# Kernel optimization log

Measured on AMD Instinct MI355X. Metric: run time of the kernel, lower is better.

Reference implementation:

```python
import jax, jax.numpy as jnp
import numpy as np

N = 100000
E = 1600000
D = 64
EPS = 1e-5


def setup_inputs() -> dict:
    key = jax.random.key(0)
    ks = jax.random.split(key, 16)
    x = jax.random.normal(ks[0], (N, D), dtype=jnp.float32)
    edge_index = jax.random.randint(ks[1], (2, E), 0, N, dtype=jnp.int64)
    s = 1.0 / np.sqrt(D)
    params = {
        'W1': jax.random.uniform(ks[2], (D, D), jnp.float32, -s, s),
        'b1': jnp.zeros((D,), jnp.float32),
        'g1': jnp.ones((D,), jnp.float32),
        'be1': jnp.zeros((D,), jnp.float32),
        'W2': jax.random.uniform(ks[3], (D, D), jnp.float32, -s, s),
        'b2': jnp.zeros((D,), jnp.float32),
        'g2': jnp.ones((D,), jnp.float32),
        'be2': jnp.zeros((D,), jnp.float32),
        'W3': jax.random.uniform(ks[4], (D, D), jnp.float32, -s, s),
        'b3': jnp.zeros((D,), jnp.float32),
    }
    return {'x': x, 'edge_index': edge_index, **params}


def _gcn_norm(edge_index):
    # add self-loops, symmetric normalization (PyG GCNConv default)
    loop = jnp.arange(N, dtype=edge_index.dtype)
    src = jnp.concatenate([edge_index[0], loop])  # [E+N]
    dst = jnp.concatenate([edge_index[1], loop])
    deg = jax.ops.segment_sum(jnp.ones_like(src, dtype=jnp.float32), dst, num_segments=N)
    dinv = jnp.where(deg > 0, jax.lax.rsqrt(deg), 0.0)
    norm = dinv[src] * dinv[dst]  # [E+N]
    return src, dst, norm


def _gcn_conv(x, src, dst, norm, W, b):
    h = x @ W                        # [N, D] transform first (PyG order)
    msg = h[src] * norm[:, None]     # gather + scale  [E+N, D]
    out = jax.ops.segment_sum(msg, dst, num_segments=N)  # scatter-add
    return out + b


def _bn(x, g, b):
    # BatchNorm1d over nodes, batch statistics (training-mode math)
    m = jnp.mean(x, axis=0)
    v = jnp.var(x, axis=0)
    return g * (x - m) * jax.lax.rsqrt(v + EPS) + b


def reference(x, edge_index, W1, b1, g1, be1, W2, b2, g2, be2, W3, b3):
    src, dst, norm = _gcn_norm(edge_index)
    h = _gcn_conv(x, src, dst, norm, W1, b1)
    h = jax.nn.relu(_bn(h, g1, be1))
    h = _gcn_conv(h, src, dst, norm, W2, b2)
    h = jax.nn.relu(_bn(h, g2, be2))
    h = _gcn_conv(h, src, dst, norm, W3, b3)
    return h
```

## Files before the change

kernel.cpp:

```cpp
#include <hip/hip_runtime.h>
#include <hip/hip_bf16.h>


#define FD 64
#define EPSF 1e-5f

#define NBUCK 256
#define BSHIFT 9
#define BWID 512
#define SLOTS 28
#define P1_EDGES 4096

typedef __attribute__((ext_vector_type(8))) short bf16x8;
typedef __attribute__((ext_vector_type(4))) float f32x4;

__device__ __forceinline__ float bf2f(ushort u) {
  return __uint_as_float((unsigned)u << 16);
}
__device__ __forceinline__ ushort f2bf_bits(float f) {
  __hip_bfloat16 h = __float2bfloat16(f);
  return *(ushort*)&h;
}

__global__ void detect64_kernel(const int* __restrict__ ei, int* __restrict__ flag) {
  int lane = threadIdx.x;
  int v = ei[2 * lane + 1];
  unsigned long long nz = __ballot(v != 0);
  if (lane == 0) *flag = (nz == 0ull) ? 1 : 0;
}

__global__ __launch_bounds__(256) void hist_kernel(const int* __restrict__ ei, int E,
                                                   const int* __restrict__ flag,
                                                   int* __restrict__ bhist) {
  __shared__ int h[NBUCK];
  const int tid = threadIdx.x;
  h[tid] = 0;
  __syncthreads();
  const int is64 = *flag;
  const int base = blockIdx.x * P1_EDGES;
#pragma unroll 1
  for (int k = 0; k < P1_EDGES / 256; ++k) {
    int e = base + k * 256 + tid;
    if (e < E) {
      int d = is64 ? ei[2 * (E + e)] : ei[E + e];
      atomicAdd(&h[d >> BSHIFT], 1);
    }
  }
  __syncthreads();
  if (h[tid]) atomicAdd(&bhist[tid], h[tid]);
}

__global__ __launch_bounds__(256) void bscan_kernel(const int* __restrict__ bhist,
                                                    int* __restrict__ bbase,
                                                    int* __restrict__ bcur) {
  __shared__ int lds[NBUCK];
  int t = threadIdx.x;
  int v = bhist[t];
  lds[t] = v;
  __syncthreads();
  for (int off = 1; off < NBUCK; off <<= 1) {
    int tv = (t >= off) ? lds[t - off] : 0;
    __syncthreads();
    lds[t] += tv;
    __syncthreads();
  }
  int ex = lds[t] - v;
  bbase[t] = ex;
  bcur[t] = ex;
}

__global__ __launch_bounds__(256) void fill1_kernel(const int* __restrict__ ei, int E,
                                                    const int* __restrict__ flag,
                                                    int* __restrict__ bcur,
                                                    int2* __restrict__ stage) {
  __shared__ int2 sbuf[NBUCK][SLOTS];
  __shared__ int scnt[NBUCK];
  __shared__ int sbase[NBUCK];
  const int tid = threadIdx.x;
  scnt[tid] = 0;
  __syncthreads();
  const int is64 = *flag;
  const int base = blockIdx.x * P1_EDGES;
#pragma unroll 1
  for (int k = 0; k < P1_EDGES / 256; ++k) {
    int e = base + k * 256 + tid;
    if (e < E) {
      int s = is64 ? ei[2 * e] : ei[e];
      int d = is64 ? ei[2 * (E + e)] : ei[E + e];
      int b = d >> BSHIFT;
      int pos = atomicAdd(&scnt[b], 1);
      if (pos < SLOTS) {
        sbuf[b][pos] = make_int2(s, d);
      } else {
        stage[atomicAdd(&bcur[b], 1)] = make_int2(s, d);
      }
    }
  }
  __syncthreads();
  {
    int c = scnt[tid];
    if (c > SLOTS) c = SLOTS;
    scnt[tid] = c;
    sbase[tid] = c ? atomicAdd(&bcur[tid], c) : 0;
  }
  __syncthreads();
  for (int idx = tid; idx < NBUCK * SLOTS; idx += 256) {
    int b = idx / SLOTS, sl = idx - b * SLOTS;
    if (sl < scnt[b]) stage[sbase[b] + sl] = sbuf[b][sl];
  }
}

__global__ __launch_bounds__(256) void degcount_kernel(const int2* __restrict__ stage,
                                                       const int* __restrict__ bbase,
                                                       const int* __restrict__ bcur,
                                                       int* __restrict__ deg,
                                                       float* __restrict__ dinv, int N) {
  __shared__ int h[BWID];
  const int b = blockIdx.x;
  const int tid = threadIdx.x;
  for (int i = tid; i < BWID; i += 256) h[i] = 0;
  __syncthreads();
  const int lo = bbase[b], hi = bcur[b];
  for (int i = lo + tid; i < hi; i += 256)
    atomicAdd(&h[stage[i].y - (b << BSHIFT)], 1);
  __syncthreads();
  const int n0 = b << BSHIFT;
  for (int i = tid; i < BWID; i += 256) {
    int node = n0 + i;
    if (node < N) {
      int d = h[i];
      deg[node] = d;
      dinv[node] = rsqrtf((float)(d + 1));
    }
  }
}

__global__ __launch_bounds__(1024) void scan1_kernel(const int* __restrict__ deg,
                                                     int* __restrict__ rowptr,
                                                     int* __restrict__ partial, int N) {
  __shared__ int lds[1024];
  int i = blockIdx.x * 1024 + threadIdx.x;
  int v = (i < N) ? deg[i] : 0;
  lds[threadIdx.x] = v;
  __syncthreads();
  for (int off = 1; off < 1024; off <<= 1) {
    int t = (threadIdx.x >= (unsigned)off) ? lds[threadIdx.x - off] : 0;
    __syncthreads();
    lds[threadIdx.x] += t;
    __syncthreads();
  }
  if (i < N) rowptr[i + 1] = lds[threadIdx.x];
  if (threadIdx.x == 1023) partial[blockIdx.x] = lds[1023];
}

__global__ __launch_bounds__(128) void scan2_kernel(int* __restrict__ partial, int B) {
  __shared__ int lds[128];
  int t = threadIdx.x;
  int v = (t < B) ? partial[t] : 0;
  lds[t] = v;
  __syncthreads();
  for (int off = 1; off < 128; off <<= 1) {
    int tv = (t >= off) ? lds[t - off] : 0;
    __syncthreads();
    lds[t] += tv;
    __syncthreads();
  }
  if (t < B) partial[t] = lds[t] - v;
}

__global__ __launch_bounds__(1024) void scan3_kernel(const int* __restrict__ deg,
                                                     int* __restrict__ rowptr,
                                                     const int* __restrict__ partial,
                                                     int* __restrict__ cursor, int N) {
  int i = blockIdx.x * 1024 + threadIdx.x;
  if (i < N) {
    int r = rowptr[i + 1] + partial[blockIdx.x];
    rowptr[i + 1] = r;
    cursor[i] = r - deg[i];
    if (i == 0) rowptr[0] = 0;
  }
}

__global__ __launch_bounds__(256) void fill2_kernel(const int2* __restrict__ stage,
                                                    const int* __restrict__ bbase,
                                                    const int* __restrict__ bcur,
                                                    int* __restrict__ cursor,
                                                    const float* __restrict__ dinv,
                                                    int2* __restrict__ colw) {
  const int b = blockIdx.x >> 1;
  const int half = blockIdx.x & 1;
  const int lo = bbase[b];
  const int hi = bcur[b];
  for (int i = lo + half * 256 + threadIdx.x; i < hi; i += 512) {
    int2 sd = stage[i];
    int slot = atomicAdd(&cursor[sd.y], 1);
    colw[slot] = make_int2(sd.x, __float_as_int(dinv[sd.x] * dinv[sd.y]));
  }
}

__global__ __launch_bounds__(256) void deg_atomic_kernel(const int* __restrict__ ei, int E,
                                                         const int* __restrict__ flag,
                                                         int* __restrict__ deg) {
  int e = blockIdx.x * 256 + threadIdx.x;
  if (e >= E) return;
  const int is64 = *flag;
  int d = is64 ? ei[2 * (E + e)] : ei[E + e];
  atomicAdd(&deg[d], 1);
}
__global__ __launch_bounds__(256) void dinv_kernel(const int* __restrict__ deg,
                                                   float* __restrict__ dinv, int N) {
  int i = blockIdx.x * 256 + threadIdx.x;
  if (i < N) dinv[i] = rsqrtf((float)(deg[i] + 1));
}
__global__ __launch_bounds__(256) void fill_direct_kernel(const int* __restrict__ ei, int E,
                                                          const int* __restrict__ flag,
                                                          const float* __restrict__ dinv,
                                                          int* __restrict__ cursor,
                                                          int2* __restrict__ colw) {
  int e = blockIdx.x * 256 + threadIdx.x;
  if (e >= E) return;
  const int is64 = *flag;
  int s = is64 ? ei[2 * e] : ei[e];
  int d = is64 ? ei[2 * (E + e)] : ei[E + e];
  int slot = atomicAdd(&cursor[d], 1);
  colw[slot] = make_int2(s, __float_as_int(dinv[s] * dinv[d]));
}

__global__ __launch_bounds__(256) void cast_kernel(const float* __restrict__ in,
                                                   ushort* __restrict__ out, int total) {
  int i = (blockIdx.x * 256 + threadIdx.x) * 4;
  if (i >= total) return;
  float4 v = *(const float4*)(in + i);
  ushort4 o;
  o.x = f2bf_bits(v.x);
  o.y = f2bf_bits(v.y);
  o.z = f2bf_bits(v.z);
  o.w = f2bf_bits(v.w);
  *(ushort4*)(out + i) = o;
}

template <bool BN>
__global__ __launch_bounds__(256) void agg_kernel(const ushort* __restrict__ H,
                                                  const int* __restrict__ rowptr,
                                                  const int2* __restrict__ colw,
                                                  const float* __restrict__ dinv,
                                                  const float* __restrict__ stats,
                                                  const float* __restrict__ g,
                                                  const float* __restrict__ be,
                                                  ushort* __restrict__ out, int N) {
  const int lane = threadIdx.x & 63;
  const int wid = threadIdx.x >> 6;
  const int dst = blockIdx.x * 4 + wid;
  if (dst >= N) return;

  float a = 1.f, c = 0.f;
  if (BN) {
    float invN = 1.0f / (float)N;
    float m = stats[lane] * invN;
    float v = stats[64 + lane] * invN - m * m;
    float r = rsqrtf(v + EPSF);
    a = g[lane] * r;
    c = be[lane] - m * a;
  }

  const float di = dinv[dst];
  float hd = bf2f(H[(size_t)dst * FD + lane]);
  if (BN) hd = fmaxf(fmaf(a, hd, c), 0.f);
  const float self = di * di * hd;

  float acc[8] = {0.f, 0.f, 0.f, 0.f, 0.f, 0.f, 0.f, 0.f};

  const int e0 = __builtin_amdgcn_readfirstlane(rowptr[dst]);
  const int e1 = __builtin_amdgcn_readfirstlane(rowptr[dst + 1]);
  for (int e = e0; e < e1; e += 8) {
#pragma unroll
    for (int u = 0; u < 8; ++u) {
      int ee = e + u;
      int idx = (ee < e1) ? ee : (e1 - 1);
      int2 cw = colw[idx];
      float w = (ee < e1) ? __int_as_float(cw.y) : 0.f;
      float h = bf2f(H[(size_t)cw.x * FD + lane]);
      if (BN) h = fmaxf(fmaf(a, h, c), 0.f);
      acc[u] = fmaf(w, h, acc[u]);
    }
  }
  float s = ((acc[0] + acc[1]) + (acc[2] + acc[3])) +
            ((acc[4] + acc[5]) + (acc[6] + acc[7])) + self;
  out[(size_t)dst * FD + lane] = f2bf_bits(s);
}

template <bool BF16OUT>
__global__ __launch_bounds__(256) void gemm_mfma_kernel(const ushort* __restrict__ A,
                                                        const float* __restrict__ W,
                                                        const float* __restrict__ bias,
                                                        ushort* __restrict__ outb,
                                                        float* __restrict__ outf,
                                                        float* __restrict__ stats, int N) {
  const int lane = threadIdx.x & 63;
  const int wid = threadIdx.x >> 6;
  const int lo = lane & 15;
  const int hi = lane >> 4;

  __shared__ float sred[128];
  if (BF16OUT) {
    if (threadIdx.x < 128) sred[threadIdx.x] = 0.f;
    __syncthreads();
  }

  bf16x8 bfrag[2][4];
#pragma unroll
  for (int kk = 0; kk < 2; ++kk)
#pragma unroll
    for (int nt = 0; nt < 4; ++nt)
#pragma unroll
      for (int j = 0; j < 8; ++j) {
        int k = kk * 32 + hi * 8 + j;
        bfrag[kk][nt][j] = (short)f2bf_bits(W[k * FD + nt * 16 + lo]);
      }

  float bl[4];
#pragma unroll
  for (int nt = 0; nt < 4; ++nt) bl[nt] = bias[nt * 16 + lo];

  float s1[4] = {0.f, 0.f, 0.f, 0.f};
  float s2[4] = {0.f, 0.f, 0.f, 0.f};

  const int TILES = (N + 15) / 16;
  const int stride = gridDim.x * 4;
  for (int tile = blockIdx.x * 4 + wid; tile < TILES; tile += stride) {
    const int row0 = tile * 16;
    const int ar = min(row0 + lo, N - 1);
    const ushort* ap = A + (size_t)ar * FD + hi * 8;
    bf16x8 a0 = *(const bf16x8*)ap;
    bf16x8 a1 = *(const bf16x8*)(ap + 32);

    f32x4 acc[4] = {{0.f, 0.f, 0.f, 0.f},
                    {0.f, 0.f, 0.f, 0.f},
                    {0.f, 0.f, 0.f, 0.f},
                    {0.f, 0.f, 0.f, 0.f}};
#pragma unroll
    for (int nt = 0; nt < 4; ++nt) {
      acc[nt] = __builtin_amdgcn_mfma_f32_16x16x32_bf16(a0, bfrag[0][nt], acc[nt], 0, 0, 0);
      acc[nt] = __builtin_amdgcn_mfma_f32_16x16x32_bf16(a1, bfrag[1][nt], acc[nt], 0, 0, 0);
    }

#pragma unroll
    for (int nt = 0; nt < 4; ++nt) {
#pragma unroll
      for (int r = 0; r < 4; ++r) {
        int row = row0 + hi * 4 + r;
        if (row < N) {
          float o = acc[nt][r] + bl[nt];
          if (BF16OUT) {
            outb[(size_t)row * FD + nt * 16 + lo] = f2bf_bits(o);
            s1[nt] += o;
            s2[nt] += o * o;
          } else {
            outf[(size_t)row * FD + nt * 16 + lo] = o;
          }
        }
      }
    }
  }

  if (BF16OUT) {
#pragma unroll
    for (int nt = 0; nt < 4; ++nt) {
      atomicAdd(&sred[nt * 16 + lo], s1[nt]);
      atomicAdd(&sred[64 + nt * 16 + lo], s2[nt]);
    }
    __syncthreads();
    if (threadIdx.x < 128) atomicAdd(&stats[threadIdx.x], sred[threadIdx.x]);
  }
}

extern "C" void kernel_launch(void* const* d_in, const int* in_sizes, int n_in,
                              void* d_out, int out_size, void* d_ws, size_t ws_size,
                              hipStream_t stream) {
  const float* x = (const float*)d_in[0];
  const int* ei = (const int*)d_in[1];
  const float* W1 = (const float*)d_in[2];
  const float* b1 = (const float*)d_in[3];
  const float* g1 = (const float*)d_in[4];
  const float* be1 = (const float*)d_in[5];
  const float* W2 = (const float*)d_in[6];
  const float* b2 = (const float*)d_in[7];
  const float* g2 = (const float*)d_in[8];
  const float* be2 = (const float*)d_in[9];
  const float* W3 = (const float*)d_in[10];
  const float* b3 = (const float*)d_in[11];

  const int N = in_sizes[0] / FD;
  const int E = in_sizes[1] / 2;
  const int nB = (N + BWID - 1) >> BSHIFT;

  char* p = (char*)d_ws;
  auto alloc = [&](size_t bytes) {
    char* r = p;
    p += (bytes + 255) & ~(size_t)255;
    return r;
  };
  int* flag = (int*)alloc(4);
  float* stats1 = (float*)alloc(128 * 4);
  float* stats2 = (float*)alloc(128 * 4);
  int* partial = (int*)alloc(128 * 4);
  int* bhist = (int*)alloc(NBUCK * 4);
  int* bbase = (int*)alloc(NBUCK * 4);
  int* bcur = (int*)alloc(NBUCK * 4);
  int* deg = (int*)alloc((size_t)N * 4);
  float* dinv = (float*)alloc((size_t)N * 4);
  int* rowptr = (int*)alloc((size_t)(N + 1) * 4);
  int* cursor = (int*)alloc((size_t)N * 4);
  int2* colw = (int2*)alloc((size_t)E * 8);
  ushort* T0 = (ushort*)alloc((size_t)N * FD * 2);
  ushort* T1 = (ushort*)alloc((size_t)N * FD * 2);
  size_t base_need = (size_t)(p - (char*)d_ws);
  int2* stage = (int2*)alloc((size_t)E * 8);
  size_t full_need = (size_t)(p - (char*)d_ws);
  const bool two_phase =
      ((ws_size == 0) || (ws_size >= full_need)) && (N <= NBUCK * BWID);
  (void)base_need;

  hipMemsetAsync(stats1, 0, 128 * 4, stream);
  hipMemsetAsync(stats2, 0, 128 * 4, stream);

  const int NB = (N + 1023) / 1024;
  const int EB = (E + P1_EDGES - 1) / P1_EDGES;

  detect64_kernel<<<1, 64, 0, stream>>>(ei, flag);

  if (two_phase) {
    hipMemsetAsync(bhist, 0, NBUCK * 4, stream);
    hist_kernel<<<EB, 256, 0, stream>>>(ei, E, flag, bhist);
    bscan_kernel<<<1, NBUCK, 0, stream>>>(bhist, bbase, bcur);
    fill1_kernel<<<EB, 256, 0, stream>>>(ei, E, flag, bcur, stage);
    degcount_kernel<<<nB, 256, 0, stream>>>(stage, bbase, bcur, deg, dinv, N);
    scan1_kernel<<<NB, 1024, 0, stream>>>(deg, rowptr, partial, N);
    scan2_kernel<<<1, 128, 0, stream>>>(partial, NB);
    scan3_kernel<<<NB, 1024, 0, stream>>>(deg, rowptr, partial, cursor, N);
    fill2_kernel<<<2 * nB, 256, 0, stream>>>(stage, bbase, bcur, cursor, dinv, colw);
  } else {
    hipMemsetAsync(deg, 0, (size_t)N * 4, stream);
    deg_atomic_kernel<<<(E + 255) / 256, 256, 0, stream>>>(ei, E, flag, deg);
    dinv_kernel<<<(N + 255) / 256, 256, 0, stream>>>(deg, dinv, N);
    scan1_kernel<<<NB, 1024, 0, stream>>>(deg, rowptr, partial, N);
    scan2_kernel<<<1, 128, 0, stream>>>(partial, NB);
    scan3_kernel<<<NB, 1024, 0, stream>>>(deg, rowptr, partial, cursor, N);
    fill_direct_kernel<<<(E + 255) / 256, 256, 0, stream>>>(ei, E, flag, dinv, cursor,
                                                            colw);
  }

  const int aggGrid = (N + 3) / 4;
  const int castGrid = (N * FD / 4 + 255) / 256;
  const int TILES = (N + 15) / 16;
  const int gemmGrid = (TILES + 15) / 16;

  cast_kernel<<<castGrid, 256, 0, stream>>>(x, T0, N * FD);
  agg_kernel<false><<<aggGrid, 256, 0, stream>>>(T0, rowptr, colw, dinv, nullptr, nullptr,
                                                 nullptr, T1, N);
  gemm_mfma_kernel<true><<<gemmGrid, 256, 0, stream>>>(T1, W1, b1, T0, nullptr, stats1, N);

  agg_kernel<true><<<aggGrid, 256, 0, stream>>>(T0, rowptr, colw, dinv, stats1, g1, be1,
                                                T1, N);
  gemm_mfma_kernel<true><<<gemmGrid, 256, 0, stream>>>(T1, W2, b2, T0, nullptr, stats2, N);

  agg_kernel<true><<<aggGrid, 256, 0, stream>>>(T0, rowptr, colw, dinv, stats2, g2, be2,
                                                T1, N);
  gemm_mfma_kernel<false><<<gemmGrid, 256, 0, stream>>>(T1, W3, b3, nullptr,
                                                        (float*)d_out, nullptr, N);
}
```

Baseline: 351.4 us.

## Aggregate four nodes per wavefront with 16 lanes each; fold memsets into init kernel

The aggregation kernel now gives each 16-lane group one destination node, with each lane loading 4 bf16 features (8 bytes) per neighbour instead of 2 bytes per lane for a whole wavefront per node. The goal is wider per-lane gathers, fewer waves, and per-group loop bounds under an __any loop. Because the four nodes in a wave have different degrees, groups that finish early sit idle until the longest row is done. The separate memsets and the detect kernel are also merged into one init kernel to cut launch overhead.

```diff
diff --git a/kernel.cpp b/kernel.cpp
--- a/kernel.cpp
+++ b/kernel.cpp
@@ -22,11 +22,22 @@
   return *(ushort*)&h;
 }
 
-__global__ void detect64_kernel(const int* __restrict__ ei, int* __restrict__ flag) {
-  int lane = threadIdx.x;
-  int v = ei[2 * lane + 1];
-  unsigned long long nz = __ballot(v != 0);
-  if (lane == 0) *flag = (nz == 0ull) ? 1 : 0;
+__global__ __launch_bounds__(256) void init_kernel(const int* __restrict__ ei,
+                                                   int* __restrict__ flag,
+                                                   int* __restrict__ bhist,
+                                                   float* __restrict__ stats1,
+                                                   float* __restrict__ stats2) {
+  int t = threadIdx.x;
+  bhist[t] = 0;
+  if (t < 128) {
+    stats1[t] = 0.f;
+    stats2[t] = 0.f;
+  }
+  if (t < 64) {
+    int v = ei[2 * t + 1];
+    unsigned long long nz = __ballot(v != 0);
+    if (t == 0) *flag = (nz == 0ull) ? 1 : 0;
+  }
 }
 
 __global__ __launch_bounds__(256) void hist_kernel(const int* __restrict__ ei, int E,
@@ -250,43 +261,89 @@
                                                   ushort* __restrict__ out, int N) {
   const int lane = threadIdx.x & 63;
   const int wid = threadIdx.x >> 6;
-  const int dst = blockIdx.x * 4 + wid;
-  if (dst >= N) return;
-
-  float a = 1.f, c = 0.f;
+  const int grp = lane >> 4;
+  const int fl = lane & 15;
+  const int dst = (blockIdx.x * 4 + wid) * 4 + grp;
+  const bool live = dst < N;
+  const int dc = live ? dst : N - 1;
+
+  float a[4], cc[4];
   if (BN) {
-    float invN = 1.0f / (float)N;
-    float m = stats[lane] * invN;
-    float v = stats[64 + lane] * invN - m * m;
-    float r = rsqrtf(v + EPSF);
-    a = g[lane] * r;
-    c = be[lane] - m * a;
-  }
-
-  const float di = dinv[dst];
-  float hd = bf2f(H[(size_t)dst * FD + lane]);
-  if (BN) hd = fmaxf(fmaf(a, hd, c), 0.f);
-  const float self = di * di * hd;
-
-  float acc[8] = {0.f, 0.f, 0.f, 0.f, 0.f, 0.f, 0.f, 0.f};
-
-  const int e0 = __builtin_amdgcn_readfirstlane(rowptr[dst]);
-  const int e1 = __builtin_amdgcn_readfirstlane(rowptr[dst + 1]);
-  for (int e = e0; e < e1; e += 8) {
-#pragma unroll
-    for (int u = 0; u < 8; ++u) {
-      int ee = e + u;
-      int idx = (ee < e1) ? ee : (e1 - 1);
-      int2 cw = colw[idx];
-      float w = (ee < e1) ? __int_as_float(cw.y) : 0.f;
-      float h = bf2f(H[(size_t)cw.x * FD + lane]);
-      if (BN) h = fmaxf(fmaf(a, h, c), 0.f);
-      acc[u] = fmaf(w, h, acc[u]);
-    }
-  }
-  float s = ((acc[0] + acc[1]) + (acc[2] + acc[3])) +
-            ((acc[4] + acc[5]) + (acc[6] + acc[7])) + self;
-  out[(size_t)dst * FD + lane] = f2bf_bits(s);
+    const float invN = 1.0f / (float)N;
+#pragma unroll
+    for (int j = 0; j < 4; ++j) {
+      int f = fl * 4 + j;
+      float m = stats[f] * invN;
+      float v = stats[64 + f] * invN - m * m;
+      float r = rsqrtf(v + EPSF);
+      a[j] = g[f] * r;
+      cc[j] = be[f] - m * a[j];
+    }
+  }
+
+  const int e0 = rowptr[dc];
+  const int e1 = live ? rowptr[dc + 1] : e0;
+  const float di = dinv[dc];
+
+  float acc[4][4];
+#pragma unroll
+  for (int u = 0; u < 4; ++u)
+#pragma unroll
+    for (int j = 0; j < 4; ++j) acc[u][j] = 0.f;
+
+  {
+    uint2 uv = *(const uint2*)(H + (size_t)dc * FD + fl * 4);
+    float h0 = __uint_as_float(uv.x << 16);
+    float h1 = __uint_as_float(uv.x & 0xffff0000u);
+    float h2 = __uint_as_float(uv.y << 16);
+    float h3 = __uint_as_float(uv.y & 0xffff0000u);
+    if (BN) {
+      h0 = fmaxf(fmaf(a[0], h0, cc[0]), 0.f);
+      h1 = fmaxf(fmaf(a[1], h1, cc[1]), 0.f);
+      h2 = fmaxf(fmaf(a[2], h2, cc[2]), 0.f);
+      h3 = fmaxf(fmaf(a[3], h3, cc[3]), 0.f);
+    }
+    const float dsq = di * di;
+    acc[0][0] = dsq * h0;
+    acc[0][1] = dsq * h1;
+    acc[0][2] = dsq * h2;
+    acc[0][3] = dsq * h3;
+  }
+
+  for (int base = e0; __any(base < e1); base += 4) {
+#pragma unroll
+    for (int u = 0; u < 4; ++u) {
+      const int ee = base + u;
+      const bool valid = ee < e1;
+      const int idx = valid ? ee : 0;
+      const int2 cw = colw[idx];
+      const float w = valid ? __int_as_float(cw.y) : 0.f;
+      uint2 uv = *(const uint2*)(H + (size_t)cw.x * FD + fl * 4);
+      float h0 = __uint_as_float(uv.x << 16);
+      float h1 = __uint_as_float(uv.x & 0xffff0000u);
+      float h2 = __uint_as_float(uv.y << 16);
+      float h3 = __uint_as_float(uv.y & 0xffff0000u);
+      if (BN) {
+        h0 = fmaxf(fmaf(a[0], h0, cc[0]), 0.f);
+        h1 = fmaxf(fmaf(a[1], h1, cc[1]), 0.f);
+        h2 = fmaxf(fmaf(a[2], h2, cc[2]), 0.f);
+        h3 = fmaxf(fmaf(a[3], h3, cc[3]), 0.f);
+      }
+      acc[u][0] = fmaf(w, h0, acc[u][0]);
+      acc[u][1] = fmaf(w, h1, acc[u][1]);
+      acc[u][2] = fmaf(w, h2, acc[u][2]);
+      acc[u][3] = fmaf(w, h3, acc[u][3]);
+    }
+  }
+
+  if (live) {
+    ushort4 o;
+    o.x = f2bf_bits((acc[0][0] + acc[1][0]) + (acc[2][0] + acc[3][0]));
+    o.y = f2bf_bits((acc[0][1] + acc[1][1]) + (acc[2][1] + acc[3][1]));
+    o.z = f2bf_bits((acc[0][2] + acc[1][2]) + (acc[2][2] + acc[3][2]));
+    o.w = f2bf_bits((acc[0][3] + acc[1][3]) + (acc[2][3] + acc[3][3]));
+    *(ushort4*)(out + (size_t)dst * FD + fl * 4) = o;
+  }
 }
 
 template <bool BF16OUT>
@@ -421,16 +478,12 @@
       ((ws_size == 0) || (ws_size >= full_need)) && (N <= NBUCK * BWID);
   (void)base_need;
 
-  hipMemsetAsync(stats1, 0, 128 * 4, stream);
-  hipMemsetAsync(stats2, 0, 128 * 4, stream);
-
   const int NB = (N + 1023) / 1024;
   const int EB = (E + P1_EDGES - 1) / P1_EDGES;
 
-  detect64_kernel<<<1, 64, 0, stream>>>(ei, flag);
+  init_kernel<<<1, 256, 0, stream>>>(ei, flag, bhist, stats1, stats2);
 
   if (two_phase) {
-    hipMemsetAsync(bhist, 0, NBUCK * 4, stream);
     hist_kernel<<<EB, 256, 0, stream>>>(ei, E, flag, bhist);
     bscan_kernel<<<1, NBUCK, 0, stream>>>(bhist, bbase, bcur);
     fill1_kernel<<<EB, 256, 0, stream>>>(ei, E, flag, bcur, stage);
@@ -450,7 +503,7 @@
                                                             colw);
   }
 
-  const int aggGrid = (N + 3) / 4;
+  const int aggGrid = (N + 15) / 16;
   const int castGrid = (N * FD / 4 + 255) / 256;
   const int TILES = (N + 15) / 16;
   const int gemmGrid = (TILES + 15) / 16;
```

Measured after the change: 317.3 us. 1.11x faster.
